# Optimization experiments

Hardware: AMD Instinct MI355X
Metric: run time of the kernel (lower is better)

## Reference

```python
import jax, jax.numpy as jnp
import numpy as np

N, S, H = 16, 2048, 1024
K = 8           # num_models (experts)
D = H // 4      # bottleneck = hidden_dim // ds_factor


def setup_inputs() -> dict:
    key = jax.random.key(0)
    k1, k2, k3, k4, k5, k6 = jax.random.split(key, 6)
    hidden_states = jax.random.normal(k1, (N, S, H), dtype=jnp.float32)
    p = jax.random.uniform(k2, (N, K), dtype=jnp.float32)
    prob = p / jnp.sum(p, axis=-1, keepdims=True)  # normalized routing probs
    std = 0.02
    w_down = jax.random.normal(k3, (K, D, H), dtype=jnp.float32) * std
    b_down = jax.random.normal(k4, (K, D), dtype=jnp.float32) * std
    w_up = jax.random.normal(k5, (K, H, D), dtype=jnp.float32) * std
    b_up = jax.random.normal(k6, (K, H), dtype=jnp.float32) * std
    return {"hidden_states": hidden_states, "prob": prob,
            "w_down": w_down, "b_down": b_down,
            "w_up": w_up, "b_up": b_up}


def merge_linear(x, prob, weight, bias):
    # weight: (K, out, in); prob: (N, K) -> per-instance merged weight (N, out, in)
    w = jnp.einsum('nk,koi->noi', prob, weight)
    b = jnp.einsum('nk,ko->no', prob, bias)
    # x: (N, S, in) -> (N, S, out); matmul with per-instance weight^T
    y = jnp.einsum('nsi,noi->nso', x, w)
    return y + b[:, None, :]


def reference(hidden_states, prob, w_down, b_down, w_up, b_up):
    # MergeAdapter forward (ln_before=False, ln_after=False, dropout=0)
    residual = merge_linear(hidden_states, prob, w_down, b_down)
    residual = jax.nn.relu(residual)
    residual = merge_linear(residual, prob, w_up, b_up)
    return hidden_states + residual
```

## Files before the change

### kernel.cpp

```cpp
#include <hip/hip_runtime.h>


typedef unsigned short u16;
typedef __bf16 bf16x8 __attribute__((ext_vector_type(8)));
typedef float f32x4 __attribute__((ext_vector_type(4)));

__device__ __forceinline__ u16 f2bf(float f) {
    union { float f; unsigned int i; } v; v.f = f;
    unsigned int r = v.i + 0x7fffu + ((v.i >> 16) & 1u);
    return (u16)(r >> 16);
}

__device__ __forceinline__ void gload_lds16(const u16* g, u16* l) {
    __builtin_amdgcn_global_load_lds(
        (const __attribute__((address_space(1))) void*)g,
        (__attribute__((address_space(3))) void*)l,
        16, 0, 0);
}

__device__ __forceinline__ void store8(u16* dst, float4 a, float4 b) {
    union { uint4 u; u16 s[8]; } cv;
    cv.s[0]=f2bf(a.x); cv.s[1]=f2bf(a.y); cv.s[2]=f2bf(a.z); cv.s[3]=f2bf(a.w);
    cv.s[4]=f2bf(b.x); cv.s[5]=f2bf(b.y); cv.s[6]=f2bf(b.z); cv.s[7]=f2bf(b.w);
    *(uint4*)dst = cv.u;
}

__global__ __launch_bounds__(256)
void merge_kernel(const float* __restrict__ prob,
                  const float* __restrict__ w_down, const float* __restrict__ b_down,
                  const float* __restrict__ w_up,   const float* __restrict__ b_up,
                  u16* __restrict__ Wd, u16* __restrict__ Wu,
                  float* __restrict__ bd, float* __restrict__ bu)
{
    __shared__ float sp[128];
    const int tid = threadIdx.x;
    if (tid < 128) sp[tid] = prob[tid];
    __syncthreads();

    const int bid = blockIdx.x;
    const int E = 256 * 1024;

    if (bid < 256) {
        int v = bid * 256 + tid;
        const bool down = (v < 32768);
        const int vv = down ? v : (v - 32768);
        const float* W = down ? w_down : w_up;
        u16* O = down ? Wd : Wu;
        const size_t e = (size_t)vv * 8;

        float wf[8][8];
        #pragma unroll
        for (int k = 0; k < 8; ++k) {
            const float4 f0 = *(const float4*)(W + (size_t)k * E + e);
            const float4 f1 = *(const float4*)(W + (size_t)k * E + e + 4);
            wf[k][0] = f0.x; wf[k][1] = f0.y; wf[k][2] = f0.z; wf[k][3] = f0.w;
            wf[k][4] = f1.x; wf[k][5] = f1.y; wf[k][6] = f1.z; wf[k][7] = f1.w;
        }
        for (int n = 0; n < 16; ++n) {
            float a[8] = {0.f,0.f,0.f,0.f,0.f,0.f,0.f,0.f};
            #pragma unroll
            for (int k = 0; k < 8; ++k) {
                const float p = sp[n * 8 + k];
                #pragma unroll
                for (int j = 0; j < 8; ++j) a[j] = fmaf(p, wf[k][j], a[j]);
            }
            union { uint4 u; u16 s[8]; } ov;
            #pragma unroll
            for (int j = 0; j < 8; ++j) ov.s[j] = f2bf(a[j]);
            *(uint4*)(O + (size_t)n * E + e) = ov.u;
        }
    } else {
        int idx = (bid - 256) * 256 + tid;
        if (idx < 16 * 256) {
            const int n = idx >> 8, d = idx & 255;
            float s = 0.f;
            #pragma unroll
            for (int k = 0; k < 8; ++k)
                s = fmaf(sp[n * 8 + k], b_down[k * 256 + d], s);
            bd[idx] = s;
        } else {
            const int i2 = idx - 4096;
            const int n = i2 >> 10, h = i2 & 1023;
            float s = 0.f;
            #pragma unroll
            for (int k = 0; k < 8; ++k)
                s = fmaf(sp[n * 8 + k], b_up[k * 1024 + h], s);
            bu[i2] = s;
        }
    }
}

__global__ __launch_bounds__(512, 2)
void fused_adapter(const float* __restrict__ x, const u16* __restrict__ Wd,
                   const u16* __restrict__ Wu, const float* __restrict__ bd,
                   const float* __restrict__ bu, float* __restrict__ out)
{
    __shared__ __align__(16) u16 lds0[32768];
    __shared__ __align__(16) u16 lds1[32768];

    const int tid  = threadIdx.x;
    const int lane = tid & 63;
    const int wave = tid >> 6;
    const int quad = lane >> 4, rl = lane & 15;
    const int rxl  = rl & 7;

    const int id = blockIdx.x;
    const int r4 = id & 15;
    const int batch = (r4 & 7) * 2 + (r4 >> 3);
    const int mblk  = id >> 4;

    const float* xb  = x  + (size_t)batch * 2048 * 1024 + (size_t)mblk * 128 * 1024;
    const u16*   Wdb = Wd + (size_t)batch * 256 * 1024;
    const u16*   Wub = Wu + (size_t)batch * 1024 * 256;
    const float* bdb = bd + batch * 256;
    const float* bub = bu + batch * 1024;
    float*       ob  = out + (size_t)batch * 2048 * 1024 + (size_t)mblk * 128 * 1024;

    const int wm1 = wave >> 2, wn1 = wave & 3;

    u16* const b0x = lds1;  u16* const b0w = lds1 + 8192;
    u16* const b1x = lds0;  u16* const b1w = lds0 + 8192;

    const int xrow = tid >> 3, xsl = tid & 7;
    const int xdst0 = (xrow * 8 + (xsl ^ (xrow & 7))) * 8;
    const int xdst1 = xdst0 + 4096;
    const int wrow  = tid >> 3;
    const int wgcol = ((tid & 7) ^ ((tid >> 3) & 7)) * 8;

    f32x4 acc1[4][4] = {};

    {
        const float4 a0 = *(const float4*)(xb + (size_t)xrow * 1024 + xsl * 8);
        const float4 a1 = *(const float4*)(xb + (size_t)xrow * 1024 + xsl * 8 + 4);
        const float4 a2 = *(const float4*)(xb + (size_t)(xrow + 64) * 1024 + xsl * 8);
        const float4 a3 = *(const float4*)(xb + (size_t)(xrow + 64) * 1024 + xsl * 8 + 4);
        #pragma unroll
        for (int r = 0; r < 4; ++r)
            gload_lds16(Wdb + (size_t)(r * 64 + wrow) * 1024 + wgcol,
                        b0w + (size_t)(r * 512 + wave * 64) * 8);
        store8(b0x + xdst0, a0, a1);
        store8(b0x + xdst1, a2, a3);
    }
    __syncthreads();

    for (int it = 0; it < 16; ++it) {
        u16* cx = (it & 1) ? b1x : b0x;
        u16* cw = (it & 1) ? b1w : b0w;
        u16* nx = (it & 1) ? b0x : b1x;
        u16* nw = (it & 1) ? b0w : b1w;
        const int k1 = (it + 1) * 64;

        float4 a0, a1, a2, a3;
        if (it < 15) {
            a0 = *(const float4*)(xb + (size_t)xrow * 1024 + k1 + xsl * 8);
            a1 = *(const float4*)(xb + (size_t)xrow * 1024 + k1 + xsl * 8 + 4);
            a2 = *(const float4*)(xb + (size_t)(xrow + 64) * 1024 + k1 + xsl * 8);
            a3 = *(const float4*)(xb + (size_t)(xrow + 64) * 1024 + k1 + xsl * 8 + 4);
            #pragma unroll
            for (int r = 0; r < 4; ++r)
                gload_lds16(Wdb + (size_t)(r * 64 + wrow) * 1024 + k1 + wgcol,
                            nw + (size_t)(r * 512 + wave * 64) * 8);
        }

        #pragma unroll
        for (int kk = 0; kk < 64; kk += 32) {
            bf16x8 av[4], bv[4];
            #pragma unroll
            for (int mi = 0; mi < 4; ++mi)
                av[mi] = *(const bf16x8*)(cx + (wm1 * 64 + mi * 16 + rl) * 64
                                          + ((kk / 8 + quad) ^ rxl) * 8);
            #pragma unroll
            for (int ni = 0; ni < 4; ++ni)
                bv[ni] = *(const bf16x8*)(cw + (wn1 * 64 + ni * 16 + rl) * 64
                                          + ((kk / 8 + quad) ^ rxl) * 8);
            #pragma unroll
            for (int mi = 0; mi < 4; ++mi)
                #pragma unroll
                for (int ni = 0; ni < 4; ++ni)
                    acc1[mi][ni] = __builtin_amdgcn_mfma_f32_16x16x32_bf16(
                        av[mi], bv[ni], acc1[mi][ni], 0, 0, 0);
        }

        if (it < 15) { store8(nx + xdst0, a0, a1); store8(nx + xdst1, a2, a3); }
        __syncthreads();
    }

    #pragma unroll
    for (int ni = 0; ni < 4; ++ni) {
        const int col = wn1 * 64 + ni * 16 + rl;
        const float bv = bdb[col];
        const int lbc = col >> 3, hi = lbc & 24, c7 = lbc & 7, cl = col & 7;
        #pragma unroll
        for (int mi = 0; mi < 4; ++mi)
            #pragma unroll
            for (int i = 0; i < 4; ++i) {
                const int row = wm1 * 64 + mi * 16 + quad * 4 + i;
                const int phys = hi | (c7 ^ (row & 7));
                lds0[row * 256 + phys * 8 + cl] =
                    f2bf(fmaxf(acc1[mi][ni][i] + bv, 0.0f));
            }
    }
    __syncthreads();

    const int wm2 = wave >> 2, wn2 = wave & 3;

    const int srow = tid >> 5, ss = tid & 31;
    const int wugcol = ((ss & 24) | ((ss & 7) ^ (srow & 7))) * 8;

    auto stage_wu = [&](int c, u16* buf) {
        #pragma unroll
        for (int rr = 0; rr < 8; ++rr)
            gload_lds16(Wub + (size_t)(c * 128 + rr * 16 + srow) * 256 + wugcol,
                        buf + (size_t)(rr * 512 + wave * 64) * 8);
    };

    stage_wu(0, lds1);

    bf16x8 af[4][8];
    #pragma unroll
    for (int mi = 0; mi < 4; ++mi) {
        const int rowb = (wm2 * 64 + mi * 16 + rl) * 256;
        #pragma unroll
        for (int t = 0; t < 8; ++t) {
            const int lb = t * 4 + quad;
            const int phys = (lb & 24) | ((lb & 7) ^ rxl);
            af[mi][t] = *(const bf16x8*)(lds0 + rowb + phys * 8);
        }
    }
    __syncthreads();

    u16* cur = lds1;
    u16* nxt = lds0;
    for (int c = 0; c < 8; ++c) {
        if (c < 7) stage_wu(c + 1, nxt);

        f32x4 acc2[4][2] = {};
        #pragma unroll
        for (int t = 0; t < 8; ++t) {
            bf16x8 bv[2];
            #pragma unroll
            for (int ni = 0; ni < 2; ++ni) {
                const int rowb = (wn2 * 32 + ni * 16 + rl) * 256;
                const int lb = t * 4 + quad;
                const int phys = (lb & 24) | ((lb & 7) ^ rxl);
                bv[ni] = *(const bf16x8*)(cur + rowb + phys * 8);
            }
            #pragma unroll
            for (int mi = 0; mi < 4; ++mi)
                #pragma unroll
                for (int ni = 0; ni < 2; ++ni)
                    acc2[mi][ni] = __builtin_amdgcn_mfma_f32_16x16x32_bf16(
                        af[mi][t], bv[ni], acc2[mi][ni], 0, 0, 0);
        }

        #pragma unroll
        for (int ni = 0; ni < 2; ++ni) {
            const int colg = c * 128 + wn2 * 32 + ni * 16 + rl;
            const float bv = bub[colg];
            #pragma unroll
            for (int mi = 0; mi < 4; ++mi)
                #pragma unroll
                for (int i = 0; i < 4; ++i) {
                    const int rowl = wm2 * 64 + mi * 16 + quad * 4 + i;
                    const size_t off = (size_t)rowl * 1024 + colg;
                    ob[off] = acc2[mi][ni][i] + bv + xb[off];
                }
        }

        if (c < 7) {
            u16* t2 = cur; cur = nxt; nxt = t2;
            __syncthreads();
        }
    }
}

extern "C" void kernel_launch(void* const* d_in, const int* in_sizes, int n_in,
                              void* d_out, int out_size, void* d_ws, size_t ws_size,
                              hipStream_t stream) {
    const float* hidden = (const float*)d_in[0];
    const float* prob   = (const float*)d_in[1];
    const float* w_down = (const float*)d_in[2];
    const float* b_down = (const float*)d_in[3];
    const float* w_up   = (const float*)d_in[4];
    const float* b_up   = (const float*)d_in[5];
    float* out = (float*)d_out;

    u16* Wd = (u16*)d_ws;
    u16* Wu = Wd + (size_t)16 * 256 * 1024;
    float* bd = (float*)(Wu + (size_t)16 * 1024 * 256);
    float* bu = bd + 16 * 256;

    merge_kernel<<<336, 256, 0, stream>>>(prob, w_down, b_down, w_up, b_up,
                                          Wd, Wu, bd, bu);

    fused_adapter<<<256, 512, 0, stream>>>(hidden, Wd, Wu, bd, bu, out);
}
```

Baseline: 335.1 us.

## Halve row tile to 64 and double grid for higher occupancy

Shrinks the per-block row tile from 128 to 64 rows, cutting LDS to 80KB per block and registers per thread, and raises launch bounds to allow more resident blocks. The grid doubles to 512 blocks so there are more blocks than CUs and more waves to hide memory latency. The up-projection stage now streams 64-column weight chunks over 16 iterations instead of 128-column chunks over 8. The trade-off is that each block reuses the merged weights over fewer rows, so weight traffic from L2 doubles, and the up-projection loop syncs twice as often.

```diff
diff --git a/kernel.cpp b/kernel.cpp
--- a/kernel.cpp
+++ b/kernel.cpp
@@ -90,13 +90,12 @@
     }
 }
 
-__global__ __launch_bounds__(512, 2)
+__global__ __launch_bounds__(512, 4)
 void fused_adapter(const float* __restrict__ x, const u16* __restrict__ Wd,
                    const u16* __restrict__ Wu, const float* __restrict__ bd,
                    const float* __restrict__ bu, float* __restrict__ out)
 {
-    __shared__ __align__(16) u16 lds0[32768];
-    __shared__ __align__(16) u16 lds1[32768];
+    __shared__ __align__(16) u16 lds[40960];
 
     const int tid  = threadIdx.x;
     const int lane = tid & 63;
@@ -105,41 +104,36 @@
     const int rxl  = rl & 7;
 
     const int id = blockIdx.x;
-    const int r4 = id & 15;
-    const int batch = (r4 & 7) * 2 + (r4 >> 3);
+    const int batch = (id & 7) * 2 + ((id >> 3) & 1);
     const int mblk  = id >> 4;
 
-    const float* xb  = x  + (size_t)batch * 2048 * 1024 + (size_t)mblk * 128 * 1024;
+    const float* xb  = x  + (size_t)batch * 2048 * 1024 + (size_t)mblk * 64 * 1024;
     const u16*   Wdb = Wd + (size_t)batch * 256 * 1024;
     const u16*   Wub = Wu + (size_t)batch * 1024 * 256;
     const float* bdb = bd + batch * 256;
     const float* bub = bu + batch * 1024;
-    float*       ob  = out + (size_t)batch * 2048 * 1024 + (size_t)mblk * 128 * 1024;
+    float*       ob  = out + (size_t)batch * 2048 * 1024 + (size_t)mblk * 64 * 1024;
 
     const int wm1 = wave >> 2, wn1 = wave & 3;
 
-    u16* const b0x = lds1;  u16* const b0w = lds1 + 8192;
-    u16* const b1x = lds0;  u16* const b1w = lds0 + 8192;
+    u16* const b0x = lds;          u16* const b0w = lds + 4096;
+    u16* const b1x = lds + 20480;  u16* const b1w = lds + 24576;
 
     const int xrow = tid >> 3, xsl = tid & 7;
-    const int xdst0 = (xrow * 8 + (xsl ^ (xrow & 7))) * 8;
-    const int xdst1 = xdst0 + 4096;
+    const int xdst = (xrow * 8 + (xsl ^ (xrow & 7))) * 8;
     const int wrow  = tid >> 3;
-    const int wgcol = ((tid & 7) ^ ((tid >> 3) & 7)) * 8;
-
-    f32x4 acc1[4][4] = {};
+    const int wgcol = ((tid & 7) ^ (wrow & 7)) * 8;
+
+    f32x4 acc1[2][4] = {};
 
     {
         const float4 a0 = *(const float4*)(xb + (size_t)xrow * 1024 + xsl * 8);
         const float4 a1 = *(const float4*)(xb + (size_t)xrow * 1024 + xsl * 8 + 4);
-        const float4 a2 = *(const float4*)(xb + (size_t)(xrow + 64) * 1024 + xsl * 8);
-        const float4 a3 = *(const float4*)(xb + (size_t)(xrow + 64) * 1024 + xsl * 8 + 4);
         #pragma unroll
         for (int r = 0; r < 4; ++r)
             gload_lds16(Wdb + (size_t)(r * 64 + wrow) * 1024 + wgcol,
                         b0w + (size_t)(r * 512 + wave * 64) * 8);
-        store8(b0x + xdst0, a0, a1);
-        store8(b0x + xdst1, a2, a3);
+        store8(b0x + xdst, a0, a1);
     }
     __syncthreads();
 
@@ -150,12 +144,10 @@
         u16* nw = (it & 1) ? b0w : b1w;
         const int k1 = (it + 1) * 64;
 
-        float4 a0, a1, a2, a3;
+        float4 a0, a1;
         if (it < 15) {
             a0 = *(const float4*)(xb + (size_t)xrow * 1024 + k1 + xsl * 8);
             a1 = *(const float4*)(xb + (size_t)xrow * 1024 + k1 + xsl * 8 + 4);
-            a2 = *(const float4*)(xb + (size_t)(xrow + 64) * 1024 + k1 + xsl * 8);
-            a3 = *(const float4*)(xb + (size_t)(xrow + 64) * 1024 + k1 + xsl * 8 + 4);
             #pragma unroll
             for (int r = 0; r < 4; ++r)
                 gload_lds16(Wdb + (size_t)(r * 64 + wrow) * 1024 + k1 + wgcol,
@@ -164,40 +156,40 @@
 
         #pragma unroll
         for (int kk = 0; kk < 64; kk += 32) {
-            bf16x8 av[4], bv[4];
-            #pragma unroll
-            for (int mi = 0; mi < 4; ++mi)
-                av[mi] = *(const bf16x8*)(cx + (wm1 * 64 + mi * 16 + rl) * 64
+            bf16x8 av[2], bv[4];
+            #pragma unroll
+            for (int mi = 0; mi < 2; ++mi)
+                av[mi] = *(const bf16x8*)(cx + (wm1 * 32 + mi * 16 + rl) * 64
                                           + ((kk / 8 + quad) ^ rxl) * 8);
             #pragma unroll
             for (int ni = 0; ni < 4; ++ni)
                 bv[ni] = *(const bf16x8*)(cw + (wn1 * 64 + ni * 16 + rl) * 64
                                           + ((kk / 8 + quad) ^ rxl) * 8);
             #pragma unroll
-            for (int mi = 0; mi < 4; ++mi)
+            for (int mi = 0; mi < 2; ++mi)
                 #pragma unroll
                 for (int ni = 0; ni < 4; ++ni)
                     acc1[mi][ni] = __builtin_amdgcn_mfma_f32_16x16x32_bf16(
                         av[mi], bv[ni], acc1[mi][ni], 0, 0, 0);
         }
 
-        if (it < 15) { store8(nx + xdst0, a0, a1); store8(nx + xdst1, a2, a3); }
+        if (it < 15) store8(nx + xdst, a0, a1);
         __syncthreads();
     }
 
     #pragma unroll
     for (int ni = 0; ni < 4; ++ni) {
         const int col = wn1 * 64 + ni * 16 + rl;
-        const float bv = bdb[col];
+        const float bval = bdb[col];
         const int lbc = col >> 3, hi = lbc & 24, c7 = lbc & 7, cl = col & 7;
         #pragma unroll
-        for (int mi = 0; mi < 4; ++mi)
+        for (int mi = 0; mi < 2; ++mi)
             #pragma unroll
             for (int i = 0; i < 4; ++i) {
-                const int row = wm1 * 64 + mi * 16 + quad * 4 + i;
+                const int row = wm1 * 32 + mi * 16 + quad * 4 + i;
                 const int phys = hi | (c7 ^ (row & 7));
-                lds0[row * 256 + phys * 8 + cl] =
-                    f2bf(fmaxf(acc1[mi][ni][i] + bv, 0.0f));
+                lds[row * 256 + phys * 8 + cl] =
+                    f2bf(fmaxf(acc1[mi][ni][i] + bval, 0.0f));
             }
     }
     __syncthreads();
@@ -209,65 +201,56 @@
 
     auto stage_wu = [&](int c, u16* buf) {
         #pragma unroll
-        for (int rr = 0; rr < 8; ++rr)
-            gload_lds16(Wub + (size_t)(c * 128 + rr * 16 + srow) * 256 + wugcol,
+        for (int rr = 0; rr < 4; ++rr)
+            gload_lds16(Wub + (size_t)(c * 64 + rr * 16 + srow) * 256 + wugcol,
                         buf + (size_t)(rr * 512 + wave * 64) * 8);
     };
 
-    stage_wu(0, lds1);
-
-    bf16x8 af[4][8];
+    stage_wu(0, lds + 16384);
+
+    bf16x8 af[2][8];
     #pragma unroll
-    for (int mi = 0; mi < 4; ++mi) {
-        const int rowb = (wm2 * 64 + mi * 16 + rl) * 256;
+    for (int mi = 0; mi < 2; ++mi) {
+        const int rowb = (wm2 * 32 + mi * 16 + rl) * 256;
         #pragma unroll
         for (int t = 0; t < 8; ++t) {
             const int lb = t * 4 + quad;
             const int phys = (lb & 24) | ((lb & 7) ^ rxl);
-            af[mi][t] = *(const bf16x8*)(lds0 + rowb + phys * 8);
-        }
-    }
-    __syncthreads();
-
-    u16* cur = lds1;
-    u16* nxt = lds0;
-    for (int c = 0; c < 8; ++c) {
-        if (c < 7) stage_wu(c + 1, nxt);
-
-        f32x4 acc2[4][2] = {};
+            af[mi][t] = *(const bf16x8*)(lds + rowb + phys * 8);
+        }
+    }
+    __syncthreads();
+
+    u16* cur = lds + 16384;
+    u16* nxt = lds;
+    for (int c = 0; c < 16; ++c) {
+        if (c < 15) stage_wu(c + 1, nxt);
+
+        f32x4 acc2[2] = {};
         #pragma unroll
         for (int t = 0; t < 8; ++t) {
-            bf16x8 bv[2];
-            #pragma unroll
-            for (int ni = 0; ni < 2; ++ni) {
-                const int rowb = (wn2 * 32 + ni * 16 + rl) * 256;
-                const int lb = t * 4 + quad;
-                const int phys = (lb & 24) | ((lb & 7) ^ rxl);
-                bv[ni] = *(const bf16x8*)(cur + rowb + phys * 8);
+            const int lb = t * 4 + quad;
+            const int phys = (lb & 24) | ((lb & 7) ^ rxl);
+            const bf16x8 bv = *(const bf16x8*)(cur + (wn2 * 16 + rl) * 256
+                                               + phys * 8);
+            #pragma unroll
+            for (int mi = 0; mi < 2; ++mi)
+                acc2[mi] = __builtin_amdgcn_mfma_f32_16x16x32_bf16(
+                    af[mi][t], bv, acc2[mi], 0, 0, 0);
+        }
+
+        const int colg = c * 64 + wn2 * 16 + rl;
+        const float bval = bub[colg];
+        #pragma unroll
+        for (int mi = 0; mi < 2; ++mi)
+            #pragma unroll
+            for (int i = 0; i < 4; ++i) {
+                const int rowl = wm2 * 32 + mi * 16 + quad * 4 + i;
+                const size_t off = (size_t)rowl * 1024 + colg;
+                ob[off] = acc2[mi][i] + bval + xb[off];
             }
-            #pragma unroll
-            for (int mi = 0; mi < 4; ++mi)
-                #pragma unroll
-                for (int ni = 0; ni < 2; ++ni)
-                    acc2[mi][ni] = __builtin_amdgcn_mfma_f32_16x16x32_bf16(
-                        af[mi][t], bv[ni], acc2[mi][ni], 0, 0, 0);
-        }
-
-        #pragma unroll
-        for (int ni = 0; ni < 2; ++ni) {
-            const int colg = c * 128 + wn2 * 32 + ni * 16 + rl;
-            const float bv = bub[colg];
-            #pragma unroll
-            for (int mi = 0; mi < 4; ++mi)
-                #pragma unroll
-                for (int i = 0; i < 4; ++i) {
-                    const int rowl = wm2 * 64 + mi * 16 + quad * 4 + i;
-                    const size_t off = (size_t)rowl * 1024 + colg;
-                    ob[off] = acc2[mi][ni][i] + bv + xb[off];
-                }
-        }
-
-        if (c < 7) {
+
+        if (c < 15) {
             u16* t2 = cur; cur = nxt; nxt = t2;
             __syncthreads();
         }
@@ -293,5 +276,5 @@
     merge_kernel<<<336, 256, 0, stream>>>(prob, w_down, b_down, w_up, b_up,
                                           Wd, Wu, bd, bu);
 
-    fused_adapter<<<256, 512, 0, stream>>>(hidden, Wd, Wu, bd, bu, out);
-}
+    fused_adapter<<<512, 512, 0, stream>>>(hidden, Wd, Wu, bd, bu, out);
+}
```

Result: faster. 320.4 us (-4.4%).
